# Performance work log

Measured on AMD Instinct MI355X. Metric: run time of the kernel, lower is better.

The kernel has to match this reference:

```python
import jax, jax.numpy as jnp
import numpy as np


def setup_inputs() -> dict:
    key = jax.random.key(0)
    k1, k2 = jax.random.split(key)
    B, N, M = 2, 8192, 8192
    source_point_cloud = jax.random.normal(k1, (B, N, 3), dtype=jnp.float32)
    target_point_cloud = jax.random.normal(k2, (B, M, 3), dtype=jnp.float32)
    return {"source_point_cloud": source_point_cloud,
            "target_point_cloud": target_point_cloud}


def reference(source_point_cloud, target_point_cloud):
    # source: [B, N, 3], target: [B, M, 3]
    s, t = source_point_cloud, target_point_cloud
    # Brute-force exact 1-NN (replaces per-batch CPU cKDTree query).
    # ||s - t||^2 = ||s||^2 + ||t||^2 - 2 s.t ; argmin unaffected by const terms per row,
    # but keep ||t||^2 since it varies over the argmin axis.
    s2 = jnp.sum(s * s, axis=-1)                       # [B, N]
    t2 = jnp.sum(t * t, axis=-1)                       # [B, M]
    dots = jnp.einsum('bnd,bmd->bnm', s, t)            # [B, N, M]
    d2 = t2[:, None, :] - 2.0 * dots                   # [B, N, M] (drop s2: row-constant)
    idx = jnp.argmin(d2, axis=-1)                      # [B, N] nearest target index
    target_points = jnp.take_along_axis(t, idx[..., None], axis=1)  # [B, N, 3]
    # MSELoss (mean over all elements) per batch, then mean over batch.
    per_batch = jnp.mean((s - target_points) ** 2, axis=(1, 2))     # [B]
    return jnp.mean(per_batch)
```

## Files before the change

kernel.cpp:

```cpp
#include <hip/hip_runtime.h>

#define BLOCK  256
#define SPT    16
#define NSLICE 256

__global__ __launch_bounds__(256) void prep_kernel(
    const float* __restrict__ tgt, float4* __restrict__ tpre,
    int M, int Mp, int total)
{
    int i = blockIdx.x * 256 + threadIdx.x;
    if (i >= total) return;
    int b = i / Mp, m = i - b * Mp;
    float x = 0.f, y = 0.f, z = 0.f, t2 = 1e30f;
    if (m < M) {
        const float* p = tgt + ((size_t)b * M + m) * 3;
        x = p[0]; y = p[1]; z = p[2];
        t2 = fmaf(x, x, fmaf(y, y, z * z));
    }
    tpre[i] = make_float4(x, y, z, t2);
}

__global__ __launch_bounds__(BLOCK) void chamfer_min_kernel(
    const float* __restrict__ src, const float4* __restrict__ tpre,
    float* __restrict__ out, int N, int Mp, int total_src, float scale)
{
    const int tid = threadIdx.x;
    const int sbase = blockIdx.x * SPT;
    const int b = (sbase < total_src) ? (sbase / N) : 0;
    const float* sb = src + (size_t)b * N * 3;
    const float4* tb = tpre + (size_t)b * Mp;

    float nsx[SPT], nsy[SPT], nsz[SPT], s2[SPT], mind[SPT];
    unsigned vmask = 0;
#pragma unroll
    for (int u = 0; u < SPT; ++u) {
        int gsi = sbase + u;
        int si  = gsi - b * N;
        bool ok = (gsi < total_src) && (si >= 0) && (si < N);
        if (ok) vmask |= (1u << u);
        float x = 0.f, y = 0.f, z = 0.f;
        if (ok) {
            x = sb[(size_t)si * 3 + 0];
            y = sb[(size_t)si * 3 + 1];
            z = sb[(size_t)si * 3 + 2];
        }
        nsx[u] = -2.f * x;  nsy[u] = -2.f * y;  nsz[u] = -2.f * z;
        s2[u]  = fmaf(x, x, fmaf(y, y, z * z));
        mind[u] = 1e30f;
    }

    const int iters = Mp / NSLICE;
#pragma unroll 4
    for (int k = 0; k < iters; k += 2) {
        float4 t0 = tb[(size_t)k * NSLICE + tid];
        float4 t1 = tb[(size_t)(k + 1) * NSLICE + tid];
#pragma unroll
        for (int u = 0; u < SPT; ++u) {
            float d0 = fmaf(nsx[u], t0.x,
                       fmaf(nsy[u], t0.y, fmaf(nsz[u], t0.z, t0.w)));
            float d1 = fmaf(nsx[u], t1.x,
                       fmaf(nsy[u], t1.y, fmaf(nsz[u], t1.z, t1.w)));
            mind[u] = fminf(mind[u], fminf(d0, d1));
        }
    }

#pragma unroll
    for (int u = 0; u < SPT; ++u) {
#pragma unroll
        for (int off = 1; off < 64; off <<= 1) {
            mind[u] = fminf(mind[u], __shfl_xor(mind[u], off, 64));
        }
    }

    __shared__ float red[BLOCK / 64][SPT];
    const int lane = tid & 63;
    const int w    = tid >> 6;
    if (lane == 0) {
#pragma unroll
        for (int u = 0; u < SPT; ++u) red[w][u] = mind[u];
    }
    __syncthreads();

    if (tid == 0) {
        float ssum = 0.f;
#pragma unroll
        for (int u = 0; u < SPT; ++u) {
            float mv = red[0][u];
#pragma unroll
            for (int ww = 1; ww < BLOCK / 64; ++ww) mv = fminf(mv, red[ww][u]);
            if (vmask & (1u << u)) ssum += s2[u] + mv;
        }
        atomicAdd(out, ssum * scale);
    }
}

extern "C" void kernel_launch(void* const* d_in, const int* in_sizes, int n_in,
                              void* d_out, int out_size, void* d_ws, size_t ws_size,
                              hipStream_t stream) {
    const float* src = (const float*)d_in[0];
    const float* tgt = (const float*)d_in[1];
    float* out = (float*)d_out;

    const int B = 2;
    const int N = in_sizes[0] / (B * 3);
    const int M = in_sizes[1] / (B * 3);
    const int total_src = B * N;

    const int Mp = ((M + 2 * NSLICE - 1) / (2 * NSLICE)) * (2 * NSLICE);
    float4* tpre = (float4*)d_ws;

    hipMemsetAsync(d_out, 0, sizeof(float), stream);

    const int prep_total = B * Mp;
    prep_kernel<<<(prep_total + 255) / 256, 256, 0, stream>>>(
        tgt, tpre, M, Mp, prep_total);

    const int grid = (total_src + SPT - 1) / SPT;
    chamfer_min_kernel<<<grid, BLOCK, 0, stream>>>(
        src, tpre, out, N, Mp, total_src,
        1.0f / (3.0f * (float)N * (float)B));
}
```

Baseline: 83.90 us.

## Vectorize distance FMAs with packed float2 and fold output zeroing into prep

The inner distance loop now pairs two target points into float2 vectors so the compiler can emit packed FMA instructions (v_pk_fma_f32 on CDNA), roughly halving the FMA instruction count. Target loads are batched eight at a time per iteration, and the padding granularity grows to match. The separate memset launch is removed by zeroing the output inside the prep kernel. The costs are higher register pressure from the duplicated source coordinates and load batching, plus more padding of the target array.

```diff
diff --git a/kernel.cpp b/kernel.cpp
--- a/kernel.cpp
+++ b/kernel.cpp
@@ -3,12 +3,16 @@
 #define BLOCK  256
 #define SPT    16
 #define NSLICE 256
+#define UN     8
+
+typedef float vfloat2 __attribute__((ext_vector_type(2)));
 
 __global__ __launch_bounds__(256) void prep_kernel(
     const float* __restrict__ tgt, float4* __restrict__ tpre,
-    int M, int Mp, int total)
+    float* __restrict__ out, int M, int Mp, int total)
 {
     int i = blockIdx.x * 256 + threadIdx.x;
+    if (i == 0) out[0] = 0.f;
     if (i >= total) return;
     int b = i / Mp, m = i - b * Mp;
     float x = 0.f, y = 0.f, z = 0.f, t2 = 1e30f;
@@ -30,7 +34,8 @@
     const float* sb = src + (size_t)b * N * 3;
     const float4* tb = tpre + (size_t)b * Mp;
 
-    float nsx[SPT], nsy[SPT], nsz[SPT], s2[SPT], mind[SPT];
+    vfloat2 nsx2[SPT], nsy2[SPT], nsz2[SPT];
+    float s2[SPT], mind[SPT];
     unsigned vmask = 0;
 #pragma unroll
     for (int u = 0; u < SPT; ++u) {
@@ -44,23 +49,33 @@
             y = sb[(size_t)si * 3 + 1];
             z = sb[(size_t)si * 3 + 2];
         }
-        nsx[u] = -2.f * x;  nsy[u] = -2.f * y;  nsz[u] = -2.f * z;
-        s2[u]  = fmaf(x, x, fmaf(y, y, z * z));
+        nsx2[u] = (vfloat2){-2.f * x, -2.f * x};
+        nsy2[u] = (vfloat2){-2.f * y, -2.f * y};
+        nsz2[u] = (vfloat2){-2.f * z, -2.f * z};
+        s2[u]   = fmaf(x, x, fmaf(y, y, z * z));
         mind[u] = 1e30f;
     }
 
-    const int iters = Mp / NSLICE;
-#pragma unroll 4
-    for (int k = 0; k < iters; k += 2) {
-        float4 t0 = tb[(size_t)k * NSLICE + tid];
-        float4 t1 = tb[(size_t)(k + 1) * NSLICE + tid];
+    const int TPT = Mp / NSLICE;
+    for (int k0 = 0; k0 < TPT; k0 += UN) {
+        float4 t[UN];
 #pragma unroll
-        for (int u = 0; u < SPT; ++u) {
-            float d0 = fmaf(nsx[u], t0.x,
-                       fmaf(nsy[u], t0.y, fmaf(nsz[u], t0.z, t0.w)));
-            float d1 = fmaf(nsx[u], t1.x,
-                       fmaf(nsy[u], t1.y, fmaf(nsz[u], t1.z, t1.w)));
-            mind[u] = fminf(mind[u], fminf(d0, d1));
+        for (int j = 0; j < UN; ++j) {
+            t[j] = tb[(size_t)(k0 + j) * NSLICE + tid];
+        }
+#pragma unroll
+        for (int j = 0; j < UN; j += 2) {
+            vfloat2 cx = {t[j].x, t[j + 1].x};
+            vfloat2 cy = {t[j].y, t[j + 1].y};
+            vfloat2 cz = {t[j].z, t[j + 1].z};
+            vfloat2 cw = {t[j].w, t[j + 1].w};
+#pragma unroll
+            for (int u = 0; u < SPT; ++u) {
+                vfloat2 d = __builtin_elementwise_fma(nsx2[u], cx,
+                            __builtin_elementwise_fma(nsy2[u], cy,
+                            __builtin_elementwise_fma(nsz2[u], cz, cw)));
+                mind[u] = fminf(mind[u], fminf(d.x, d.y));
+            }
         }
     }
 
@@ -106,14 +121,13 @@
     const int M = in_sizes[1] / (B * 3);
     const int total_src = B * N;
 
-    const int Mp = ((M + 2 * NSLICE - 1) / (2 * NSLICE)) * (2 * NSLICE);
+    const int step = NSLICE * UN;
+    const int Mp = ((M + step - 1) / step) * step;
     float4* tpre = (float4*)d_ws;
-
-    hipMemsetAsync(d_out, 0, sizeof(float), stream);
 
     const int prep_total = B * Mp;
     prep_kernel<<<(prep_total + 255) / 256, 256, 0, stream>>>(
-        tgt, tpre, M, Mp, prep_total);
+        tgt, tpre, out, M, Mp, prep_total);
 
     const int grid = (total_src + SPT - 1) / SPT;
     chamfer_min_kernel<<<grid, BLOCK, 0, stream>>>(
```

Result: faster. 77.30 us (-7.9%).

## Split targets across blocks with SoA broadcast loads and separate min reduction

Applied to the files above, without the earlier changes.

Target points are stored as structure-of-arrays and each thread now handles one source point against a chunk of targets, with 32 target chunks spread over blocks. Wave-uniform loads and packed two-wide FMAs replace the per-thread 16-source register tiling. Partial minima go to workspace and a third kernel reduces them and accumulates the loss. The output zeroing is folded into the prep kernel instead of a memset. This trades register reuse of each loaded target for more parallelism and cheaper broadcast loads, at the cost of extra partial-result traffic and a third launch.

```diff
diff --git a/kernel.cpp b/kernel.cpp
--- a/kernel.cpp
+++ b/kernel.cpp
@@ -1,96 +1,111 @@
 #include <hip/hip_runtime.h>
 
 #define BLOCK  256
-#define SPT    16
-#define NSLICE 256
+#define TSPLIT 32
+
+typedef float vfloat2 __attribute__((ext_vector_type(2)));
 
 __global__ __launch_bounds__(256) void prep_kernel(
-    const float* __restrict__ tgt, float4* __restrict__ tpre,
-    int M, int Mp, int total)
+    const float* __restrict__ tgt, float* __restrict__ soa,
+    float* __restrict__ out, int M, int Mp, int BMp)
 {
     int i = blockIdx.x * 256 + threadIdx.x;
-    if (i >= total) return;
+    if (i == 0) out[0] = 0.f;
+    if (i >= BMp) return;
     int b = i / Mp, m = i - b * Mp;
-    float x = 0.f, y = 0.f, z = 0.f, t2 = 1e30f;
+    float x = 0.f, y = 0.f, z = 0.f, w = 1e30f;
     if (m < M) {
         const float* p = tgt + ((size_t)b * M + m) * 3;
         x = p[0]; y = p[1]; z = p[2];
-        t2 = fmaf(x, x, fmaf(y, y, z * z));
+        w = fmaf(x, x, fmaf(y, y, z * z));
     }
-    tpre[i] = make_float4(x, y, z, t2);
+    soa[i]           = x;
+    soa[BMp + i]     = y;
+    soa[2 * BMp + i] = z;
+    soa[3 * BMp + i] = w;
 }
 
-__global__ __launch_bounds__(BLOCK) void chamfer_min_kernel(
-    const float* __restrict__ src, const float4* __restrict__ tpre,
-    float* __restrict__ out, int N, int Mp, int total_src, float scale)
+__global__ __launch_bounds__(BLOCK, 8) void nn_chunk_kernel(
+    const float* __restrict__ src, const float* __restrict__ soa,
+    float* __restrict__ partial, int N, int Mp, int BMp, int SGB, int BN)
 {
     const int tid = threadIdx.x;
-    const int sbase = blockIdx.x * SPT;
-    const int b = (sbase < total_src) ? (sbase / N) : 0;
-    const float* sb = src + (size_t)b * N * 3;
-    const float4* tb = tpre + (size_t)b * Mp;
+    const int c   = blockIdx.x % TSPLIT;
+    const int sgg = blockIdx.x / TSPLIT;
+    const int b   = sgg / SGB;
+    const int sgl = sgg - b * SGB;
+    const int si  = sgl * BLOCK + tid;
 
-    float nsx[SPT], nsy[SPT], nsz[SPT], s2[SPT], mind[SPT];
-    unsigned vmask = 0;
-#pragma unroll
-    for (int u = 0; u < SPT; ++u) {
-        int gsi = sbase + u;
-        int si  = gsi - b * N;
-        bool ok = (gsi < total_src) && (si >= 0) && (si < N);
-        if (ok) vmask |= (1u << u);
-        float x = 0.f, y = 0.f, z = 0.f;
-        if (ok) {
-            x = sb[(size_t)si * 3 + 0];
-            y = sb[(size_t)si * 3 + 1];
-            z = sb[(size_t)si * 3 + 2];
-        }
-        nsx[u] = -2.f * x;  nsy[u] = -2.f * y;  nsz[u] = -2.f * z;
-        s2[u]  = fmaf(x, x, fmaf(y, y, z * z));
-        mind[u] = 1e30f;
+    float x = 0.f, y = 0.f, z = 0.f;
+    if (si < N) {
+        const float* p = src + ((size_t)b * N + si) * 3;
+        x = p[0]; y = p[1]; z = p[2];
+    }
+    const vfloat2 nsx = {-2.f * x, -2.f * x};
+    const vfloat2 nsy = {-2.f * y, -2.f * y};
+    const vfloat2 nsz = {-2.f * z, -2.f * z};
+    float mind = 1e30f;
+
+    const int CHT = Mp / TSPLIT;
+    const int f2b = (b * Mp + c * CHT) >> 1;
+    const vfloat2* __restrict__ TX = (const vfloat2*)soa;
+    const vfloat2* __restrict__ TY = (const vfloat2*)(soa + BMp);
+    const vfloat2* __restrict__ TZ = (const vfloat2*)(soa + 2 * BMp);
+    const vfloat2* __restrict__ TW = (const vfloat2*)(soa + 3 * BMp);
+
+#pragma unroll 8
+    for (int k = 0; k < CHT / 2; ++k) {
+        vfloat2 x01 = TX[f2b + k];
+        vfloat2 y01 = TY[f2b + k];
+        vfloat2 z01 = TZ[f2b + k];
+        vfloat2 w01 = TW[f2b + k];
+        vfloat2 e = x01 * nsx;
+        e = __builtin_elementwise_fma(y01, nsy, e);
+        e = __builtin_elementwise_fma(z01, nsz, e);
+        vfloat2 d = e + w01;
+        mind = fminf(mind, fminf(d.x, d.y));
     }
 
-    const int iters = Mp / NSLICE;
-#pragma unroll 4
-    for (int k = 0; k < iters; k += 2) {
-        float4 t0 = tb[(size_t)k * NSLICE + tid];
-        float4 t1 = tb[(size_t)(k + 1) * NSLICE + tid];
+    if (si < N) {
+        partial[(size_t)c * BN + (size_t)b * N + si] = mind;
+    }
+}
+
+__global__ __launch_bounds__(BLOCK) void reduce_kernel(
+    const float* __restrict__ src, const float* __restrict__ partial,
+    float* __restrict__ out, int BN, float scale)
+{
+    const int i = blockIdx.x * BLOCK + threadIdx.x;
+    float v = 0.f;
+    if (i < BN) {
+        float m0 = 1e30f, m1 = 1e30f, m2 = 1e30f, m3 = 1e30f;
 #pragma unroll
-        for (int u = 0; u < SPT; ++u) {
-            float d0 = fmaf(nsx[u], t0.x,
-                       fmaf(nsy[u], t0.y, fmaf(nsz[u], t0.z, t0.w)));
-            float d1 = fmaf(nsx[u], t1.x,
-                       fmaf(nsy[u], t1.y, fmaf(nsz[u], t1.z, t1.w)));
-            mind[u] = fminf(mind[u], fminf(d0, d1));
+        for (int c = 0; c < TSPLIT; c += 4) {
+            m0 = fminf(m0, partial[(size_t)(c + 0) * BN + i]);
+            m1 = fminf(m1, partial[(size_t)(c + 1) * BN + i]);
+            m2 = fminf(m2, partial[(size_t)(c + 2) * BN + i]);
+            m3 = fminf(m3, partial[(size_t)(c + 3) * BN + i]);
         }
+        float x = src[(size_t)i * 3 + 0];
+        float y = src[(size_t)i * 3 + 1];
+        float z = src[(size_t)i * 3 + 2];
+        v = fmaf(x, x, fmaf(y, y, z * z))
+          + fminf(fminf(m0, m1), fminf(m2, m3));
     }
 
 #pragma unroll
-    for (int u = 0; u < SPT; ++u) {
+    for (int off = 32; off > 0; off >>= 1) v += __shfl_xor(v, off, 64);
+
+    __shared__ float wsum[BLOCK / 64];
+    const int lane = threadIdx.x & 63;
+    const int w    = threadIdx.x >> 6;
+    if (lane == 0) wsum[w] = v;
+    __syncthreads();
+    if (threadIdx.x == 0) {
+        float s = 0.f;
 #pragma unroll
-        for (int off = 1; off < 64; off <<= 1) {
-            mind[u] = fminf(mind[u], __shfl_xor(mind[u], off, 64));
-        }
-    }
-
-    __shared__ float red[BLOCK / 64][SPT];
-    const int lane = tid & 63;
-    const int w    = tid >> 6;
-    if (lane == 0) {
-#pragma unroll
-        for (int u = 0; u < SPT; ++u) red[w][u] = mind[u];
-    }
-    __syncthreads();
-
-    if (tid == 0) {
-        float ssum = 0.f;
-#pragma unroll
-        for (int u = 0; u < SPT; ++u) {
-            float mv = red[0][u];
-#pragma unroll
-            for (int ww = 1; ww < BLOCK / 64; ++ww) mv = fminf(mv, red[ww][u]);
-            if (vmask & (1u << u)) ssum += s2[u] + mv;
-        }
-        atomicAdd(out, ssum * scale);
+        for (int k = 0; k < BLOCK / 64; ++k) s += wsum[k];
+        atomicAdd(out, s * scale);
     }
 }
 
@@ -104,19 +119,22 @@
     const int B = 2;
     const int N = in_sizes[0] / (B * 3);
     const int M = in_sizes[1] / (B * 3);
-    const int total_src = B * N;
+    const int BN = B * N;
 
-    const int Mp = ((M + 2 * NSLICE - 1) / (2 * NSLICE)) * (2 * NSLICE);
-    float4* tpre = (float4*)d_ws;
+    const int step = TSPLIT * 16;
+    const int Mp  = ((M + step - 1) / step) * step;
+    const int BMp = B * Mp;
 
-    hipMemsetAsync(d_out, 0, sizeof(float), stream);
+    float* soa     = (float*)d_ws;
+    float* partial = soa + 4 * (size_t)BMp;
 
-    const int prep_total = B * Mp;
-    prep_kernel<<<(prep_total + 255) / 256, 256, 0, stream>>>(
-        tgt, tpre, M, Mp, prep_total);
+    prep_kernel<<<(BMp + 255) / 256, 256, 0, stream>>>(tgt, soa, out, M, Mp, BMp);
 
-    const int grid = (total_src + SPT - 1) / SPT;
-    chamfer_min_kernel<<<grid, BLOCK, 0, stream>>>(
-        src, tpre, out, N, Mp, total_src,
-        1.0f / (3.0f * (float)N * (float)B));
+    const int SGB = (N + BLOCK - 1) / BLOCK;
+    const int grid1 = B * SGB * TSPLIT;
+    nn_chunk_kernel<<<grid1, BLOCK, 0, stream>>>(src, soa, partial,
+                                                 N, Mp, BMp, SGB, BN);
+
+    reduce_kernel<<<(BN + BLOCK - 1) / BLOCK, BLOCK, 0, stream>>>(
+        src, partial, out, BN, 1.0f / (3.0f * (float)N * (float)B));
 }
```

Result: faster. 73.21 us (-12.7%).
